# Kernel optimization log

Hardware: AMD Instinct MI355X
Metric: run time of the kernel (lower is better)

The kernel has to match this reference:

```python
import jax, jax.numpy as jnp
import numpy as np

N_NODES = 50000
N_EDGES = 800000
H = 128
FF = 4 * H
SCALE = 30.0
EPS = 1e-5


def _layer_norm(x, g, b):
    mu = jnp.mean(x, axis=-1, keepdims=True)
    var = jnp.mean((x - mu) ** 2, axis=-1, keepdims=True)
    return (x - mu) * jax.lax.rsqrt(var + EPS) * g + b


def _linear(x, W, b):
    return x @ W.T + b


def setup_inputs() -> dict:
    key = jax.random.key(0)
    ks = jax.random.split(key, 16)
    s = lambda fan_in: 1.0 / np.sqrt(fan_in)
    inp = {
        "h_V": jax.random.normal(ks[0], (N_NODES, H), jnp.float32),
        "h_E": jax.random.normal(ks[1], (N_EDGES, H), jnp.float32),
        "src_idx": jax.random.randint(ks[2], (N_EDGES,), 0, N_NODES),
        "batch_id": jnp.zeros((N_NODES,), jnp.int32),
        "dst_idx": jax.random.randint(ks[3], (N_EDGES,), 0, N_NODES),
        "W1": jax.random.uniform(ks[4], (H, 3 * H), jnp.float32, -s(3 * H), s(3 * H)),
        "b1": jnp.zeros((H,), jnp.float32),
        "W2": jax.random.uniform(ks[5], (H, H), jnp.float32, -s(H), s(H)),
        "b2": jnp.zeros((H,), jnp.float32),
        "W3": jax.random.uniform(ks[6], (H, H), jnp.float32, -s(H), s(H)),
        "b3": jnp.zeros((H,), jnp.float32),
        "ln1_g": jnp.ones((H,), jnp.float32),
        "ln1_b": jnp.zeros((H,), jnp.float32),
        "ln2_g": jnp.ones((H,), jnp.float32),
        "ln2_b": jnp.zeros((H,), jnp.float32),
        "W_in": jax.random.uniform(ks[7], (FF, H), jnp.float32, -s(H), s(H)),
        "b_in": jnp.zeros((FF,), jnp.float32),
        "W_out": jax.random.uniform(ks[8], (H, FF), jnp.float32, -s(FF), s(FF)),
        "b_out": jnp.zeros((H,), jnp.float32),
    }
    return inp


def reference(h_V, h_E, src_idx, batch_id, dst_idx,
              W1, b1, W2, b2, W3, b3,
              ln1_g, ln1_b, ln2_g, ln2_b,
              W_in, b_in, W_out, b_out):
    # gather + concat: [E, 3H]
    h_EV = jnp.concatenate([h_V[src_idx], h_E, h_V[dst_idx]], axis=-1)
    # 3-layer edge MLP (exact GELU, matching torch default)
    h = jax.nn.gelu(_linear(h_EV, W1, b1), approximate=False)
    h = jax.nn.gelu(_linear(h, W2, b2), approximate=False)
    h_message = _linear(h, W3, b3)
    # scatter_mean by src_idx over N_NODES segments
    seg_sum = jax.ops.segment_sum(h_message, src_idx, num_segments=N_NODES)
    cnt = jax.ops.segment_sum(jnp.ones((h_message.shape[0],), h_message.dtype),
                              src_idx, num_segments=N_NODES)
    dh = seg_sum / jnp.maximum(cnt, 1.0)[:, None] / SCALE
    # residual + norm (dropout = identity in eval)
    h_V = _layer_norm(h_V + dh, ln1_g, ln1_b)
    # FFN
    dh = _linear(jax.nn.gelu(_linear(h_V, W_in, b_in), approximate=False), W_out, b_out)
    h_V = _layer_norm(h_V + dh, ln2_g, ln2_b)
    return h_V
```

## Files before the change

### kernel.cpp

```cpp
#include <hip/hip_runtime.h>

#define NE 800000
#define NN 50000
#define HD 128
#define FFD 512

typedef __bf16 bf16;
typedef bf16 bf16x8 __attribute__((ext_vector_type(8)));
typedef float f32x4 __attribute__((ext_vector_type(4)));

__device__ __forceinline__ float gelu_f(float x) {
    return 0.5f * x * (1.0f + erff(x * 0.70710678118654752f));
}

__device__ __forceinline__ bf16x8 cvt8(f32x4 a, f32x4 b) {
    bf16x8 t;
    t[0] = (bf16)a[0]; t[1] = (bf16)a[1]; t[2] = (bf16)a[2]; t[3] = (bf16)a[3];
    t[4] = (bf16)b[0]; t[5] = (bf16)b[1]; t[6] = (bf16)b[2]; t[7] = (bf16)b[3];
    return t;
}

__global__ void cvt_weights(const float* __restrict__ W1, const float* __restrict__ W2,
                            const float* __restrict__ W3, const float* __restrict__ Win,
                            const float* __restrict__ Wout, bf16* __restrict__ o) {
    int i = blockIdx.x * 256 + threadIdx.x;
    if (i < 49152)        o[i] = (bf16)W1[i];
    else if (i < 65536)   o[i] = (bf16)W2[i - 49152];
    else if (i < 81920)   o[i] = (bf16)W3[i - 65536];
    else if (i < 147456)  o[i] = (bf16)Win[i - 81920];
    else if (i < 212992)  o[i] = (bf16)Wout[i - 147456];
}

__global__ void hist_kernel(const int* __restrict__ src, int* __restrict__ cnt) {
    int i = blockIdx.x * 256 + threadIdx.x;
    if (i < NE) atomicAdd(cnt + src[i], 1);
}

__global__ __launch_bounds__(256, 2) void edge_mlp(
    const float* __restrict__ hV, const float* __restrict__ hE,
    const int* __restrict__ src, const int* __restrict__ dst,
    const bf16* __restrict__ W1b, const bf16* __restrict__ W2b, const bf16* __restrict__ W3b,
    const float* __restrict__ b1, const float* __restrict__ b2, const float* __restrict__ b3,
    float* __restrict__ segsum)
{
    __shared__ bf16 lx[128][136];
    const int tid  = threadIdx.x;
    const int wave = tid >> 6, lane = tid & 63;
    const int wr = wave >> 1, wc = wave & 1;
    const int quad = lane >> 4, l16 = lane & 15;
    const int row0 = blockIdx.x * 128;

    int arow[4], asrc[4], adst[4];
#pragma unroll
    for (int rt = 0; rt < 4; ++rt) {
        int r = row0 + wr * 64 + rt * 16 + l16;
        arow[rt] = r; asrc[rt] = src[r]; adst[rt] = dst[r];
    }

    f32x4 acc[4][4];
#pragma unroll
    for (int i = 0; i < 4; ++i)
#pragma unroll
        for (int j = 0; j < 4; ++j) acc[i][j] = (f32x4){0.f, 0.f, 0.f, 0.f};

#pragma unroll
    for (int ks = 0; ks < 12; ++ks) {
        const int k = ks * 32 + quad * 8;
        bf16x8 a[4];
#pragma unroll
        for (int rt = 0; rt < 4; ++rt) {
            const float* p;
            if (ks < 4)      p = hV + (size_t)asrc[rt] * HD + k;
            else if (ks < 8) p = hE + (size_t)arow[rt] * HD + (k - 128);
            else             p = hV + (size_t)adst[rt] * HD + (k - 256);
            f32x4 f0 = *(const f32x4*)p;
            f32x4 f1 = *(const f32x4*)(p + 4);
            a[rt] = cvt8(f0, f1);
        }
        bf16x8 b[4];
#pragma unroll
        for (int ct = 0; ct < 4; ++ct) {
            int col = wc * 64 + ct * 16 + l16;
            b[ct] = *(const bf16x8*)(W1b + (size_t)col * 384 + ks * 32 + quad * 8);
        }
#pragma unroll
        for (int rt = 0; rt < 4; ++rt)
#pragma unroll
            for (int ct = 0; ct < 4; ++ct)
                acc[rt][ct] = __builtin_amdgcn_mfma_f32_16x16x32_bf16(a[rt], b[ct], acc[rt][ct], 0, 0, 0);
    }

#pragma unroll
    for (int ct = 0; ct < 4; ++ct) {
        int col = wc * 64 + ct * 16 + l16;
        float bias = b1[col];
#pragma unroll
        for (int rt = 0; rt < 4; ++rt)
#pragma unroll
            for (int r = 0; r < 4; ++r)
                lx[wr * 64 + rt * 16 + quad * 4 + r][col] = (bf16)gelu_f(acc[rt][ct][r] + bias);
    }
    __syncthreads();

#pragma unroll
    for (int i = 0; i < 4; ++i)
#pragma unroll
        for (int j = 0; j < 4; ++j) acc[i][j] = (f32x4){0.f, 0.f, 0.f, 0.f};
#pragma unroll
    for (int ks = 0; ks < 4; ++ks) {
        bf16x8 a[4], b[4];
#pragma unroll
        for (int rt = 0; rt < 4; ++rt)
            a[rt] = *(const bf16x8*)&lx[wr * 64 + rt * 16 + l16][ks * 32 + quad * 8];
#pragma unroll
        for (int ct = 0; ct < 4; ++ct)
            b[ct] = *(const bf16x8*)(W2b + (size_t)(wc * 64 + ct * 16 + l16) * HD + ks * 32 + quad * 8);
#pragma unroll
        for (int rt = 0; rt < 4; ++rt)
#pragma unroll
            for (int ct = 0; ct < 4; ++ct)
                acc[rt][ct] = __builtin_amdgcn_mfma_f32_16x16x32_bf16(a[rt], b[ct], acc[rt][ct], 0, 0, 0);
    }
    __syncthreads();

#pragma unroll
    for (int ct = 0; ct < 4; ++ct) {
        int col = wc * 64 + ct * 16 + l16;
        float bias = b2[col];
#pragma unroll
        for (int rt = 0; rt < 4; ++rt)
#pragma unroll
            for (int r = 0; r < 4; ++r)
                lx[wr * 64 + rt * 16 + quad * 4 + r][col] = (bf16)gelu_f(acc[rt][ct][r] + bias);
    }
    __syncthreads();

#pragma unroll
    for (int i = 0; i < 4; ++i)
#pragma unroll
        for (int j = 0; j < 4; ++j) acc[i][j] = (f32x4){0.f, 0.f, 0.f, 0.f};
#pragma unroll
    for (int ks = 0; ks < 4; ++ks) {
        bf16x8 a[4], b[4];
#pragma unroll
        for (int rt = 0; rt < 4; ++rt)
            a[rt] = *(const bf16x8*)&lx[wr * 64 + rt * 16 + l16][ks * 32 + quad * 8];
#pragma unroll
        for (int ct = 0; ct < 4; ++ct)
            b[ct] = *(const bf16x8*)(W3b + (size_t)(wc * 64 + ct * 16 + l16) * HD + ks * 32 + quad * 8);
#pragma unroll
        for (int rt = 0; rt < 4; ++rt)
#pragma unroll
            for (int ct = 0; ct < 4; ++ct)
                acc[rt][ct] = __builtin_amdgcn_mfma_f32_16x16x32_bf16(a[rt], b[ct], acc[rt][ct], 0, 0, 0);
    }

    float b3c[4];
#pragma unroll
    for (int ct = 0; ct < 4; ++ct) b3c[ct] = b3[wc * 64 + ct * 16 + l16];
#pragma unroll
    for (int rt = 0; rt < 4; ++rt)
#pragma unroll
        for (int r = 0; r < 4; ++r) {
            int row = row0 + wr * 64 + rt * 16 + quad * 4 + r;
            float* basep = segsum + (size_t)src[row] * HD;
#pragma unroll
            for (int ct = 0; ct < 4; ++ct)
                atomicAdd(basep + wc * 64 + ct * 16 + l16, acc[rt][ct][r] + b3c[ct]);
        }
}

__global__ __launch_bounds__(256, 2) void node_ffn(
    const float* __restrict__ hV, float* __restrict__ out ,
    const int* __restrict__ cnt,
    const bf16* __restrict__ Winb, const bf16* __restrict__ Woutb,
    const float* __restrict__ bin, const float* __restrict__ bout,
    const float* __restrict__ g1, const float* __restrict__ be1,
    const float* __restrict__ g2, const float* __restrict__ be2)
{
    __shared__ bf16 lx[128][136];
    __shared__ bf16 ly[128][72];
    __shared__ float ps[128][2], pq[128][2];
    const int tid  = threadIdx.x;
    const int wave = tid >> 6, lane = tid & 63;
    const int wr = wave >> 1, wc = wave & 1;
    const int quad = lane >> 4, l16 = lane & 15;
    const int base = blockIdx.x * 128;

    for (int r = 0; r < 32; ++r) {
        int rl = wave * 32 + r;
        int node = base + rl;
        float u0 = 0.f, u1 = 0.f;
        bool valid = node < NN;
        if (valid) {
            int c = cnt[node];
            float inv = 1.0f / (30.0f * (float)(c > 1 ? c : 1));
            const float2 h = *(const float2*)(hV  + (size_t)node * HD + 2 * lane);
            const float2 s = *(const float2*)(out + (size_t)node * HD + 2 * lane);
            u0 = h.x + s.x * inv;
            u1 = h.y + s.y * inv;
        }
        float sm = u0 + u1, sq = u0 * u0 + u1 * u1;
#pragma unroll
        for (int m = 1; m < 64; m <<= 1) {
            sm += __shfl_xor(sm, m, 64);
            sq += __shfl_xor(sq, m, 64);
        }
        float mean = sm * (1.0f / 128.0f);
        float var  = sq * (1.0f / 128.0f) - mean * mean;
        float rstd = rsqrtf(var + 1e-5f);
        int c0 = 2 * lane;
        float x0 = valid ? ((u0 - mean) * rstd * g1[c0]     + be1[c0])     : 0.f;
        float x1 = valid ? ((u1 - mean) * rstd * g1[c0 + 1] + be1[c0 + 1]) : 0.f;
        lx[rl][c0] = (bf16)x0; lx[rl][c0 + 1] = (bf16)x1;
    }
    __syncthreads();

    f32x4 oacc[4][4];
#pragma unroll
    for (int i = 0; i < 4; ++i)
#pragma unroll
        for (int j = 0; j < 4; ++j) oacc[i][j] = (f32x4){0.f, 0.f, 0.f, 0.f};

    for (int c = 0; c < 8; ++c) {
        f32x4 a1[4][2];
#pragma unroll
        for (int i = 0; i < 4; ++i)
#pragma unroll
            for (int j = 0; j < 2; ++j) a1[i][j] = (f32x4){0.f, 0.f, 0.f, 0.f};
#pragma unroll
        for (int ks = 0; ks < 4; ++ks) {
            bf16x8 a[4], b[2];
#pragma unroll
            for (int rt = 0; rt < 4; ++rt)
                a[rt] = *(const bf16x8*)&lx[wr * 64 + rt * 16 + l16][ks * 32 + quad * 8];
#pragma unroll
            for (int ct = 0; ct < 2; ++ct) {
                int f = c * 64 + wc * 32 + ct * 16 + l16;
                b[ct] = *(const bf16x8*)(Winb + (size_t)f * HD + ks * 32 + quad * 8);
            }
#pragma unroll
            for (int rt = 0; rt < 4; ++rt)
#pragma unroll
                for (int ct = 0; ct < 2; ++ct)
                    a1[rt][ct] = __builtin_amdgcn_mfma_f32_16x16x32_bf16(a[rt], b[ct], a1[rt][ct], 0, 0, 0);
        }
        __syncthreads();
#pragma unroll
        for (int ct = 0; ct < 2; ++ct) {
            int f  = c * 64 + wc * 32 + ct * 16 + l16;
            int fl = wc * 32 + ct * 16 + l16;
            float bias = bin[f];
#pragma unroll
            for (int rt = 0; rt < 4; ++rt)
#pragma unroll
                for (int r = 0; r < 4; ++r)
                    ly[wr * 64 + rt * 16 + quad * 4 + r][fl] = (bf16)gelu_f(a1[rt][ct][r] + bias);
        }
        __syncthreads();
#pragma unroll
        for (int ks = 0; ks < 2; ++ks) {
            bf16x8 a[4], b[4];
#pragma unroll
            for (int rt = 0; rt < 4; ++rt)
                a[rt] = *(const bf16x8*)&ly[wr * 64 + rt * 16 + l16][ks * 32 + quad * 8];
#pragma unroll
            for (int ct = 0; ct < 4; ++ct) {
                int o = wc * 64 + ct * 16 + l16;
                b[ct] = *(const bf16x8*)(Woutb + (size_t)o * FFD + c * 64 + ks * 32 + quad * 8);
            }
#pragma unroll
            for (int rt = 0; rt < 4; ++rt)
#pragma unroll
                for (int ct = 0; ct < 4; ++ct)
                    oacc[rt][ct] = __builtin_amdgcn_mfma_f32_16x16x32_bf16(a[rt], b[ct], oacc[rt][ct], 0, 0, 0);
        }
    }

    float bo[4];
#pragma unroll
    for (int ct = 0; ct < 4; ++ct) bo[ct] = bout[wc * 64 + ct * 16 + l16];
#pragma unroll
    for (int rt = 0; rt < 4; ++rt)
#pragma unroll
        for (int r = 0; r < 4; ++r) {
            int rl = wr * 64 + rt * 16 + quad * 4 + r;
            float sm = 0.f, sq = 0.f;
#pragma unroll
            for (int ct = 0; ct < 4; ++ct) {
                int o = wc * 64 + ct * 16 + l16;
                float zz = oacc[rt][ct][r] + bo[ct] + (float)lx[rl][o];
                oacc[rt][ct][r] = zz;
                sm += zz; sq += zz * zz;
            }
#pragma unroll
            for (int m = 1; m < 16; m <<= 1) {
                sm += __shfl_xor(sm, m, 64);
                sq += __shfl_xor(sq, m, 64);
            }
            if (l16 == 0) { ps[rl][wc] = sm; pq[rl][wc] = sq; }
        }
    __syncthreads();
#pragma unroll
    for (int rt = 0; rt < 4; ++rt)
#pragma unroll
        for (int r = 0; r < 4; ++r) {
            int rl = wr * 64 + rt * 16 + quad * 4 + r;
            int node = base + rl;
            float S = ps[rl][0] + ps[rl][1];
            float Q = pq[rl][0] + pq[rl][1];
            float mean = S * (1.0f / 128.0f);
            float var  = Q * (1.0f / 128.0f) - mean * mean;
            float rstd = rsqrtf(var + 1e-5f);
            if (node < NN) {
#pragma unroll
                for (int ct = 0; ct < 4; ++ct) {
                    int o = wc * 64 + ct * 16 + l16;
                    out[(size_t)node * HD + o] = (oacc[rt][ct][r] - mean) * rstd * g2[o] + be2[o];
                }
            }
        }
}

extern "C" void kernel_launch(void* const* d_in, const int* in_sizes, int n_in,
                              void* d_out, int out_size, void* d_ws, size_t ws_size,
                              hipStream_t stream) {
    const float* hV   = (const float*)d_in[0];
    const float* hE   = (const float*)d_in[1];
    const int*   src  = (const int*)d_in[2];
    const int*   dst  = (const int*)d_in[4];
    const float* W1   = (const float*)d_in[5];
    const float* b1   = (const float*)d_in[6];
    const float* W2   = (const float*)d_in[7];
    const float* b2   = (const float*)d_in[8];
    const float* W3   = (const float*)d_in[9];
    const float* b3   = (const float*)d_in[10];
    const float* g1   = (const float*)d_in[11];
    const float* be1  = (const float*)d_in[12];
    const float* g2   = (const float*)d_in[13];
    const float* be2  = (const float*)d_in[14];
    const float* Win  = (const float*)d_in[15];
    const float* bin  = (const float*)d_in[16];
    const float* Wout = (const float*)d_in[17];
    const float* bout = (const float*)d_in[18];

    float* out = (float*)d_out;
    bf16*  wbf = (bf16*)d_ws;
    int*   cnt = (int*)((char*)d_ws + 425984);

    hipMemsetAsync(d_out, 0, (size_t)NN * HD * sizeof(float), stream);
    hipMemsetAsync(cnt, 0, NN * sizeof(int), stream);

    cvt_weights<<<832, 256, 0, stream>>>(W1, W2, W3, Win, Wout, wbf);
    hist_kernel<<<(NE + 255) / 256, 256, 0, stream>>>(src, cnt);
    edge_mlp<<<NE / 128, 256, 0, stream>>>(hV, hE, src, dst,
                                           wbf, wbf + 49152, wbf + 65536,
                                           b1, b2, b3, out);
    node_ffn<<<(NN + 127) / 128, 256, 0, stream>>>(hV, out, cnt,
                                                   wbf + 81920, wbf + 147456,
                                                   bin, bout, g1, be1, g2, be2);
}
```

Measured before the change: 1.337 ms.

## Sort edges by source via counting sort and segment-reduce before atomics

New measurement: 1.385 ms. 1.04x slower.

```diff
diff --git a/kernel.cpp b/kernel.cpp
--- a/kernel.cpp
+++ b/kernel.cpp
@@ -36,25 +36,78 @@
     if (i < NE) atomicAdd(cnt + src[i], 1);
 }
 
+__global__ __launch_bounds__(1024) void scan_kernel(const int* __restrict__ cnt,
+                                                    int* __restrict__ head) {
+    __shared__ int wsum[16];
+    __shared__ int carry;
+    const int tid = threadIdx.x, lane = tid & 63, w = tid >> 6;
+    if (tid == 0) carry = 0;
+    __syncthreads();
+    for (int base = 0; base < NN; base += 1024) {
+        int i = base + tid;
+        int v = (i < NN) ? cnt[i] : 0;
+        int x = v;
+#pragma unroll
+        for (int m = 1; m < 64; m <<= 1) {
+            int y = __shfl_up(x, m, 64);
+            if (lane >= m) x += y;
+        }
+        if (lane == 63) wsum[w] = x;
+        __syncthreads();
+        if (w == 0) {
+            int s = (lane < 16) ? wsum[lane] : 0;
+#pragma unroll
+            for (int m = 1; m < 16; m <<= 1) {
+                int y = __shfl_up(s, m, 64);
+                if (lane >= m) s += y;
+            }
+            if (lane < 16) wsum[lane] = s;
+        }
+        __syncthreads();
+        int excl = carry + (w > 0 ? wsum[w - 1] : 0) + x - v;
+        if (i < NN) head[i] = excl;
+        int total = wsum[15];
+        __syncthreads();
+        if (tid == 0) carry += total;
+        __syncthreads();
+    }
+}
+
+__global__ void scatter_perm(const int* __restrict__ src, int* __restrict__ head,
+                             int* __restrict__ perm) {
+    int i = blockIdx.x * 256 + threadIdx.x;
+    if (i < NE) {
+        int pos = atomicAdd(head + src[i], 1);
+        perm[pos] = i;
+    }
+}
+
 __global__ __launch_bounds__(256, 2) void edge_mlp(
     const float* __restrict__ hV, const float* __restrict__ hE,
     const int* __restrict__ src, const int* __restrict__ dst,
+    const int* __restrict__ perm,
     const bf16* __restrict__ W1b, const bf16* __restrict__ W2b, const bf16* __restrict__ W3b,
     const float* __restrict__ b1, const float* __restrict__ b2, const float* __restrict__ b3,
     float* __restrict__ segsum)
 {
-    __shared__ bf16 lx[128][136];
+    __shared__ __align__(16) char smem[128 * 132 * 4];
+    bf16  (*lx)[136] = (bf16 (*)[136])smem;
+    float (*lz)[132] = (float (*)[132])smem;
+    __shared__ int ssrc[128];
+
     const int tid  = threadIdx.x;
     const int wave = tid >> 6, lane = tid & 63;
     const int wr = wave >> 1, wc = wave & 1;
     const int quad = lane >> 4, l16 = lane & 15;
     const int row0 = blockIdx.x * 128;
 
+    if (tid < 128) ssrc[tid] = src[perm[row0 + tid]];
+
     int arow[4], asrc[4], adst[4];
 #pragma unroll
     for (int rt = 0; rt < 4; ++rt) {
-        int r = row0 + wr * 64 + rt * 16 + l16;
-        arow[rt] = r; asrc[rt] = src[r]; adst[rt] = dst[r];
+        int e = perm[row0 + wr * 64 + rt * 16 + l16];
+        arow[rt] = e; asrc[rt] = src[e]; adst[rt] = dst[e];
     }
 
     f32x4 acc[4][4];
@@ -154,20 +207,38 @@
             for (int ct = 0; ct < 4; ++ct)
                 acc[rt][ct] = __builtin_amdgcn_mfma_f32_16x16x32_bf16(a[rt], b[ct], acc[rt][ct], 0, 0, 0);
     }
+    __syncthreads();
 
     float b3c[4];
 #pragma unroll
     for (int ct = 0; ct < 4; ++ct) b3c[ct] = b3[wc * 64 + ct * 16 + l16];
 #pragma unroll
-    for (int rt = 0; rt < 4; ++rt)
-#pragma unroll
-        for (int r = 0; r < 4; ++r) {
-            int row = row0 + wr * 64 + rt * 16 + quad * 4 + r;
-            float* basep = segsum + (size_t)src[row] * HD;
-#pragma unroll
-            for (int ct = 0; ct < 4; ++ct)
-                atomicAdd(basep + wc * 64 + ct * 16 + l16, acc[rt][ct][r] + b3c[ct]);
-        }
+    for (int ct = 0; ct < 4; ++ct)
+#pragma unroll
+        for (int rt = 0; rt < 4; ++rt)
+#pragma unroll
+            for (int r = 0; r < 4; ++r)
+                lz[wr * 64 + rt * 16 + quad * 4 + r][wc * 64 + ct * 16 + l16] =
+                    acc[rt][ct][r] + b3c[ct];
+    __syncthreads();
+
+    {
+        const int c = tid & 127, h = tid >> 7;
+        const int rbeg = h * 64, rend = rbeg + 64;
+        float sum = lz[rbeg][c];
+        int cur = ssrc[rbeg];
+        for (int r = rbeg + 1; r < rend; ++r) {
+            int s = ssrc[r];
+            float v = lz[r][c];
+            if (s != cur) {
+                atomicAdd(segsum + (size_t)cur * HD + c, sum);
+                cur = s; sum = v;
+            } else {
+                sum += v;
+            }
+        }
+        atomicAdd(segsum + (size_t)cur * HD + c, sum);
+    }
 }
 
 __global__ __launch_bounds__(256, 2) void node_ffn(
@@ -345,15 +416,19 @@
     const float* bout = (const float*)d_in[18];
 
     float* out = (float*)d_out;
-    bf16*  wbf = (bf16*)d_ws;
-    int*   cnt = (int*)((char*)d_ws + 425984);
+    bf16* wbf  = (bf16*)d_ws;
+    int*  cnt  = (int*)((char*)d_ws + 425984);
+    int*  head = (int*)((char*)d_ws + 625984);
+    int*  perm = (int*)((char*)d_ws + 825984);
 
     hipMemsetAsync(d_out, 0, (size_t)NN * HD * sizeof(float), stream);
     hipMemsetAsync(cnt, 0, NN * sizeof(int), stream);
 
     cvt_weights<<<832, 256, 0, stream>>>(W1, W2, W3, Win, Wout, wbf);
     hist_kernel<<<(NE + 255) / 256, 256, 0, stream>>>(src, cnt);
-    edge_mlp<<<NE / 128, 256, 0, stream>>>(hV, hE, src, dst,
+    scan_kernel<<<1, 1024, 0, stream>>>(cnt, head);
+    scatter_perm<<<(NE + 255) / 256, 256, 0, stream>>>(src, head, perm);
+    edge_mlp<<<NE / 128, 256, 0, stream>>>(hV, hE, src, dst, perm,
                                            wbf, wbf + 49152, wbf + 65536,
                                            b1, b2, b3, out);
     node_ffn<<<(NN + 127) / 128, 256, 0, stream>>>(hV, out, cnt,
```
